# Optimization experiments

Hardware: AMD Instinct MI355X
Metric: run time of the kernel (lower is better)

## Reference

```python
import jax, jax.numpy as jnp
import numpy as np
import math

H, NH, NKV, HD, FF = 1024, 16, 4, 64, 4096
B, S = 2, 2048
EPS, THETA = 1e-6, 10000.0


def _rmsnorm(x, w, eps=EPS):
    v = jnp.mean(x.astype(jnp.float32) ** 2, axis=-1, keepdims=True)
    return (x.astype(jnp.float32) * jax.lax.rsqrt(v + eps)).astype(x.dtype) * w


def _rope_tables(seq_len, head_dim, theta=THETA):
    inv_freq = 1.0 / (theta ** (jnp.arange(0, head_dim, 2, dtype=jnp.float32) / head_dim))
    freqs = jnp.arange(seq_len, dtype=jnp.float32)[:, None] * inv_freq[None, :]
    emb = jnp.concatenate([freqs, freqs], axis=-1)  # [S, HD]
    return jnp.cos(emb), jnp.sin(emb)


def _rotate_half(x):
    x1, x2 = jnp.split(x, 2, axis=-1)
    return jnp.concatenate([-x2, x1], axis=-1)


def _apply_rope(x, cos, sin):
    # x: [B, h, S, HD]; cos/sin: [S, HD] broadcast over batch/heads
    return x * cos[None, None] + _rotate_half(x) * sin[None, None]


def setup_inputs() -> dict:
    key = jax.random.key(0)
    ks = jax.random.split(key, 12)
    std = 0.02
    return {
        "hidden_states": jax.random.normal(ks[0], (B, S, H), jnp.float32),
        "kv_states": jax.random.normal(ks[1], (B, S, H), jnp.float32),
        "attention_mask": jnp.zeros((B, 1, S, S), jnp.float32),
        "ln1_w": jnp.ones((H,), jnp.float32),
        "ln2_w": jnp.ones((H,), jnp.float32),
        "Wq": jax.random.normal(ks[2], (H, NH * HD), jnp.float32) * std,
        "Wk": jax.random.normal(ks[3], (H, NKV * HD), jnp.float32) * std,
        "Wv": jax.random.normal(ks[4], (H, NKV * HD), jnp.float32) * std,
        "Wo": jax.random.normal(ks[5], (NH * HD, H), jnp.float32) * std,
        "Wgate": jax.random.normal(ks[6], (H, FF), jnp.float32) * std,
        "Wup": jax.random.normal(ks[7], (H, FF), jnp.float32) * std,
        "Wdown": jax.random.normal(ks[8], (FF, H), jnp.float32) * std,
    }


def reference(hidden_states, kv_states, attention_mask, ln1_w, ln2_w,
              Wq, Wk, Wv, Wo, Wgate, Wup, Wdown):
    bsz, q_len, _ = hidden_states.shape
    k_len = kv_states.shape[1]

    residual = hidden_states
    h = _rmsnorm(hidden_states, ln1_w)   # input_layernorm on queries
    kv = _rmsnorm(kv_states, ln1_w)      # same norm applied to kv_states

    q = (h @ Wq).reshape(bsz, q_len, NH, HD).transpose(0, 2, 1, 3)    # [B,NH,Sq,HD]
    k = (kv @ Wk).reshape(bsz, k_len, NKV, HD).transpose(0, 2, 1, 3)  # [B,NKV,Sk,HD]
    v = (kv @ Wv).reshape(bsz, k_len, NKV, HD).transpose(0, 2, 1, 3)

    cos_q, sin_q = _rope_tables(q_len, HD)
    cos_k, sin_k = _rope_tables(k_len, HD)
    q = _apply_rope(q, cos_q, sin_q)
    k = _apply_rope(k, cos_k, sin_k)

    # repeat_kv: GQA expand to NH heads
    groups = NH // NKV
    k = jnp.repeat(k, groups, axis=1)
    v = jnp.repeat(v, groups, axis=1)

    scores = jnp.einsum("bhqd,bhkd->bhqk", q, k) / math.sqrt(HD)
    scores = scores + attention_mask  # additive mask [B,1,Sq,Sk]
    probs = jax.nn.softmax(scores.astype(jnp.float32), axis=-1).astype(q.dtype)
    attn = jnp.einsum("bhqk,bhkd->bhqd", probs, v)
    attn = attn.transpose(0, 2, 1, 3).reshape(bsz, q_len, NH * HD)
    attn = attn @ Wo

    hidden = residual + attn

    residual = hidden
    x = _rmsnorm(hidden, ln2_w)
    x = (jax.nn.silu(x @ Wgate) * (x @ Wup)) @ Wdown  # SwiGLU MLP
    return residual + x
```

## Files before the change

### kernel.cpp

```cpp
#include <hip/hip_runtime.h>
#include <math.h>

#define SS 2048

typedef __attribute__((ext_vector_type(8))) short s16x8;
typedef __attribute__((ext_vector_type(4))) float f32x4;
typedef __attribute__((ext_vector_type(16))) float f32x16;

__device__ __forceinline__ unsigned short f2bf(float f) {
  union { float f; unsigned u; } a; a.f = f;
  unsigned r = a.u + 0x7fffu + ((a.u >> 16) & 1u);
  return (unsigned short)(r >> 16);
}
__device__ __forceinline__ float bf2f(unsigned short b) {
  union { unsigned u; float f; } a; a.u = ((unsigned)b) << 16;
  return a.f;
}
__device__ __forceinline__ unsigned cvtpk(float a, float b) {
  unsigned d; asm("v_cvt_pk_bf16_f32 %0, %1, %2" : "=v"(d) : "v"(a), "v"(b)); return d;
}
__device__ __forceinline__ float fexp2(float x) {
  float r; asm("v_exp_f32 %0, %1" : "=v"(r) : "v"(x)); return r;
}
__device__ __forceinline__ void async16(void* lds, const void* g) {
  __builtin_amdgcn_global_load_lds(
      (const __attribute__((address_space(1))) unsigned int*)g,
      (__attribute__((address_space(3))) unsigned int*)lds, 16, 0, 0);
}
__device__ __forceinline__ f32x4 mfma_bf16(s16x8 a, s16x8 b, f32x4 c) {
  return __builtin_amdgcn_mfma_f32_16x16x32_bf16(a, b, c, 0, 0, 0);
}
__device__ __forceinline__ f32x16 mfma32(s16x8 a, s16x8 b, f32x16 c) {
  return __builtin_amdgcn_mfma_f32_32x32x16_bf16(a, b, c, 0, 0, 0);
}
__device__ __forceinline__ void xcd_swz(int& bx, int& by) {
  int nx = gridDim.x;
  int nwg = nx * gridDim.y;
  int bid = blockIdx.y * nx + blockIdx.x;
  int sid = (bid & 7) * (nwg >> 3) + (bid >> 3);
  bx = sid % nx; by = sid / nx;
}

__global__ __launch_bounds__(256) void k_transpose(const float* __restrict__ W,
                                                   const float* __restrict__ W2,
                                                   unsigned short* __restrict__ WT,
                                                   unsigned short* __restrict__ WT2,
                                                   int K, int N) {
  const float* Wp = blockIdx.z ? W2 : W;
  unsigned short* WTp = blockIdx.z ? WT2 : WT;
  __shared__ float tile[32][33];
  int t = threadIdx.x;
  int tx = t & 31, ty = t >> 5;
  int n0 = blockIdx.x * 32, k0 = blockIdx.y * 32;
#pragma unroll
  for (int i = 0; i < 4; ++i)
    tile[ty + 8 * i][tx] = Wp[(size_t)(k0 + ty + 8 * i) * N + n0 + tx];
  __syncthreads();
#pragma unroll
  for (int i = 0; i < 4; ++i)
    WTp[(size_t)(n0 + ty + 8 * i) * K + k0 + tx] = f2bf(tile[tx][ty + 8 * i]);
}

__global__ __launch_bounds__(256) void k_vtrans(const unsigned short* __restrict__ QKV,
                                                unsigned short* __restrict__ VT) {
  __shared__ unsigned short tile[32][33];
  int t = threadIdx.x, tx = t & 31, ty = t >> 5;
  int s0 = blockIdx.x * 32, d0 = blockIdx.y * 32;
  int bk = blockIdx.z; int b = bk >> 2, kvh = bk & 3;
#pragma unroll
  for (int i = 0; i < 4; ++i)
    tile[ty + 8 * i][tx] =
        QKV[((size_t)b * SS + s0 + ty + 8 * i) * 1536 + 1280 + kvh * 64 + d0 + tx];
  __syncthreads();
#pragma unroll
  for (int i = 0; i < 4; ++i)
    VT[((size_t)bk * 64 + d0 + ty + 8 * i) * SS + s0 + tx] = tile[tx][ty + 8 * i];
}

__global__ void k_rope_tables(float* __restrict__ cosT, float* __restrict__ sinT) {
  int idx = blockIdx.x * 256 + threadIdx.x;
  int s = idx >> 5, i = idx & 31;
  double ang = (double)s * pow(10000.0, -(double)(2 * i) / 64.0);
  cosT[idx] = (float)cos(ang);
  sinT[idx] = (float)sin(ang);
}

__global__ __launch_bounds__(256) void k_rmsnorm(const float* __restrict__ X,
                                                 const float* __restrict__ X2,
                                                 const float* __restrict__ Wt,
                                                 unsigned short* __restrict__ Y,
                                                 unsigned short* __restrict__ Y2) {
  int row = blockIdx.x, t = threadIdx.x;
  const float* Xp = X;
  unsigned short* Yp = Y;
  if (X2 && row >= 4096) { Xp = X2; Yp = Y2; row -= 4096; }
  float4 v = ((const float4*)Xp)[(size_t)row * 256 + t];
  float ssq = v.x * v.x + v.y * v.y + v.z * v.z + v.w * v.w;
#pragma unroll
  for (int m = 1; m < 64; m <<= 1) ssq += __shfl_xor(ssq, m);
  __shared__ float red[4];
  if ((t & 63) == 0) red[t >> 6] = ssq;
  __syncthreads();
  float sc = rsqrtf((red[0] + red[1] + red[2] + red[3]) * (1.0f / 1024.0f) + 1e-6f);
  float4 wv = ((const float4*)Wt)[t];
  ushort4 o;
  o.x = f2bf(v.x * sc * wv.x); o.y = f2bf(v.y * sc * wv.y);
  o.z = f2bf(v.z * sc * wv.z); o.w = f2bf(v.w * sc * wv.w);
  ((ushort4*)Yp)[(size_t)row * 256 + t] = o;
}

__global__ __launch_bounds__(256) void k_rope(unsigned short* __restrict__ X,
                                              const float* __restrict__ cosT,
                                              const float* __restrict__ sinT,
                                              int stride, int hbase) {
  int idx = blockIdx.x * 256 + threadIdx.x;
  int seg = idx & 7, tok = idx >> 3;
  int head = blockIdx.y + hbase;
  int s = tok & (SS - 1);
  int d0 = seg * 4;
  unsigned short* p = X + (size_t)tok * stride + head * 64;
  ushort4 lo = *(ushort4*)&p[d0];
  ushort4 hi = *(ushort4*)&p[d0 + 32];
  float4 cs = *(const float4*)&cosT[s * 32 + d0];
  float4 sn = *(const float4*)&sinT[s * 32 + d0];
  ushort4 olo, ohi;
  olo.x = f2bf(bf2f(lo.x) * cs.x - bf2f(hi.x) * sn.x);
  olo.y = f2bf(bf2f(lo.y) * cs.y - bf2f(hi.y) * sn.y);
  olo.z = f2bf(bf2f(lo.z) * cs.z - bf2f(hi.z) * sn.z);
  olo.w = f2bf(bf2f(lo.w) * cs.w - bf2f(hi.w) * sn.w);
  ohi.x = f2bf(bf2f(hi.x) * cs.x + bf2f(lo.x) * sn.x);
  ohi.y = f2bf(bf2f(hi.y) * cs.y + bf2f(lo.y) * sn.y);
  ohi.z = f2bf(bf2f(hi.z) * cs.z + bf2f(lo.z) * sn.z);
  ohi.w = f2bf(bf2f(hi.w) * cs.w + bf2f(lo.w) * sn.w);
  *(ushort4*)&p[d0] = olo;
  *(ushort4*)&p[d0 + 32] = ohi;
}

template <int EPI, int BN>
__global__ __launch_bounds__(256) void k_gemm(const unsigned short* __restrict__ A,
                                              const unsigned short* __restrict__ BT,
                                              int K, int ldc,
                                              unsigned short* Cb,
                                              float* __restrict__ Cf,
                                              const float* __restrict__ Res) {
  constexpr int NW = BN / 32;
  __shared__ __align__(16) unsigned short at[128 * 32];
  __shared__ __align__(16) unsigned short bt[BN * 32];
  int bx, by; xcd_swz(bx, by);
  int t = threadIdx.x, w = t >> 6, l = t & 63;
  int g = l >> 4, c = l & 15;
  int wm = w >> 1, wn = w & 1;
  f32x4 acc[4][NW] = {};
  const unsigned short* gA = A + (size_t)(by * 128 + (t >> 2)) * K + (t & 3) * 8;
  const unsigned short* gB = BT + (size_t)(bx * BN + (t >> 2)) * K + (t & 3) * 8;
  unsigned short* dA = &at[w * 512];
  unsigned short* dB = &bt[w * 512];
  const int nk = K >> 5;
  for (int kt = 0; kt < nk; ++kt) {
    async16(dA, gA);
    async16(dA + 2048, gA + (size_t)64 * K);
    async16(dB, gB);
    if (BN == 128) async16(dB + 2048, gB + (size_t)64 * K);
    gA += 32; gB += 32;
    __syncthreads();
    s16x8 af[4], bfr[NW];
#pragma unroll
    for (int m = 0; m < 4; ++m) af[m] = *(const s16x8*)&at[(wm * 64 + m * 16 + c) * 32 + g * 8];
#pragma unroll
    for (int n = 0; n < NW; ++n)
      bfr[n] = *(const s16x8*)&bt[(wn * (BN / 2) + n * 16 + c) * 32 + g * 8];
#pragma unroll
    for (int m = 0; m < 4; ++m)
#pragma unroll
      for (int n = 0; n < NW; ++n)
        acc[m][n] = mfma_bf16(af[m], bfr[n], acc[m][n]);
    __syncthreads();
  }
  size_t rb = (size_t)by * 128 + wm * 64;
  size_t cbase = (size_t)bx * BN + wn * (BN / 2);
#pragma unroll
  for (int m = 0; m < 4; ++m)
#pragma unroll
    for (int n = 0; n < NW; ++n)
#pragma unroll
      for (int r = 0; r < 4; ++r) {
        size_t row = rb + m * 16 + g * 4 + r;
        size_t col = cbase + n * 16 + c;
        float v = acc[m][n][r];
        if (EPI == 0) Cb[row * ldc + col] = f2bf(v);
        else Cf[row * ldc + col] = v + Res[row * ldc + col];
      }
}

__global__ __launch_bounds__(512) void k_gateup(const unsigned short* __restrict__ A,
                                                const unsigned short* __restrict__ BTg,
                                                const unsigned short* __restrict__ BTu,
                                                unsigned short* __restrict__ Cb) {
  __shared__ __align__(16) unsigned short at[128 * 32];
  __shared__ __align__(16) unsigned short bg[128 * 32];
  __shared__ __align__(16) unsigned short bu[128 * 32];
  int bx, by; xcd_swz(bx, by);
  int t = threadIdx.x, w = t >> 6, l = t & 63;
  int g = l >> 4, c = l & 15;
  int wm = w >> 2, wn = w & 3;
  f32x4 ag[4][2] = {}, au[4][2] = {};
  const unsigned short* gA = A + (size_t)(by * 128 + (t >> 2)) * 1024 + (t & 3) * 8;
  const unsigned short* gG = BTg + (size_t)(bx * 128 + (t >> 2)) * 1024 + (t & 3) * 8;
  const unsigned short* gU = BTu + (size_t)(bx * 128 + (t >> 2)) * 1024 + (t & 3) * 8;
  unsigned short* dA = &at[w * 512];
  unsigned short* dG = &bg[w * 512];
  unsigned short* dU = &bu[w * 512];
  for (int kt = 0; kt < 32; ++kt) {
    async16(dA, gA);
    async16(dG, gG);
    async16(dU, gU);
    gA += 32; gG += 32; gU += 32;
    __syncthreads();
    s16x8 af[4], bgf[2], buf_[2];
#pragma unroll
    for (int m = 0; m < 4; ++m) af[m] = *(const s16x8*)&at[(wm * 64 + m * 16 + c) * 32 + g * 8];
#pragma unroll
    for (int n = 0; n < 2; ++n) {
      bgf[n] = *(const s16x8*)&bg[(wn * 32 + n * 16 + c) * 32 + g * 8];
      buf_[n] = *(const s16x8*)&bu[(wn * 32 + n * 16 + c) * 32 + g * 8];
    }
#pragma unroll
    for (int m = 0; m < 4; ++m)
#pragma unroll
      for (int n = 0; n < 2; ++n) {
        ag[m][n] = mfma_bf16(af[m], bgf[n], ag[m][n]);
        au[m][n] = mfma_bf16(af[m], buf_[n], au[m][n]);
      }
    __syncthreads();
  }
  size_t rb = (size_t)by * 128 + wm * 64;
  size_t cb = (size_t)bx * 128 + wn * 32;
#pragma unroll
  for (int m = 0; m < 4; ++m)
#pragma unroll
    for (int n = 0; n < 2; ++n)
#pragma unroll
      for (int r = 0; r < 4; ++r) {
        size_t row = rb + m * 16 + g * 4 + r;
        size_t col = cb + n * 16 + c;
        float gv = ag[m][n][r], uv = au[m][n][r];
        Cb[row * 4096 + col] = f2bf(gv / (1.0f + __expf(-gv)) * uv);
      }
}

__global__ __launch_bounds__(256) void k_attn(const unsigned short* __restrict__ Q,
                                              const unsigned short* __restrict__ K,
                                              const unsigned short* __restrict__ VT,
                                              const float* __restrict__ mask,
                                              const float* __restrict__ cosT,
                                              const float* __restrict__ sinT,
                                              unsigned short* __restrict__ Out) {
  __shared__ __align__(16) unsigned short Ks[2][64 * 64];
  __shared__ __align__(16) unsigned short VTs[2][64 * 64];
  const float LOG2E = 1.44269504f;
  const float SCL2 = 0.125f * 1.44269504f;
  int t = threadIdx.x, w = t >> 6, l = t & 63;
  int q32 = l & 31, hi = l >> 5;
  int blk = blockIdx.x;
  int qt = blk & 63, kvh = (blk >> 6) & 3, b = blk >> 8;
  int head = kvh * 4 + w;
  size_t tokQ = (size_t)b * SS + qt * 32;

  s16x8 qfr[4];
#pragma unroll
  for (int d = 0; d < 4; ++d)
    qfr[d] = *(const s16x8*)&Q[(tokQ + q32) * 1536 + head * 64 + d * 16 + hi * 8];
  {
    int sp = qt * 32 + q32;
    const float* ct = cosT + sp * 32;
    const float* st = sinT + sp * 32;
#pragma unroll
    for (int d = 0; d < 2; ++d) {
      unsigned wlo[4], whi[4];
#pragma unroll
      for (int j = 0; j < 8; j += 2) {
        int f0 = d * 16 + hi * 8 + j;
        float c0 = ct[f0], s0_ = st[f0];
        float c1 = ct[f0 + 1], s1_ = st[f0 + 1];
        float lo0 = bf2f((unsigned short)qfr[d][j]);
        float hi0 = bf2f((unsigned short)qfr[d + 2][j]);
        float lo1 = bf2f((unsigned short)qfr[d][j + 1]);
        float hi1 = bf2f((unsigned short)qfr[d + 2][j + 1]);
        wlo[j >> 1] = cvtpk(lo0 * c0 - hi0 * s0_, lo1 * c1 - hi1 * s1_);
        whi[j >> 1] = cvtpk(hi0 * c0 + lo0 * s0_, hi1 * c1 + lo1 * s1_);
      }
      union { unsigned u[4]; s16x8 v; } a, b2;
#pragma unroll
      for (int i = 0; i < 4; ++i) { a.u[i] = wlo[i]; b2.u[i] = whi[i]; }
      qfr[d] = a.v;
      qfr[d + 2] = b2.v;
    }
  }
  const s16x8 one8 = {(short)0x3F80, (short)0x3F80, (short)0x3F80, (short)0x3F80,
                      (short)0x3F80, (short)0x3F80, (short)0x3F80, (short)0x3F80};

  int id0 = t, id1 = t + 256;
  int row0 = id0 >> 3, b80 = id0 & 7;
  int row1 = id1 >> 3, b81 = id1 & 7;
  int so0 = row0 * 64 + ((b80 ^ (row0 & 7)) << 3);
  int so1 = row1 * 64 + ((b81 ^ (row1 & 7)) << 3);
  const unsigned short* gK = K + (size_t)b * SS * 1536 + kvh * 64;
  const unsigned short* gV = VT + (size_t)(b * 4 + kvh) * 64 * SS;

  int4 rK0 = *(const int4*)(gK + (size_t)row0 * 1536 + b80 * 8);
  int4 rK1 = *(const int4*)(gK + (size_t)row1 * 1536 + b81 * 8);
  int4 rV0 = *(const int4*)(gV + (size_t)row0 * SS + b80 * 8);
  int4 rV1 = *(const int4*)(gV + (size_t)row1 * SS + b81 * 8);
  *(int4*)&Ks[0][so0] = rK0; *(int4*)&Ks[0][so1] = rK1;
  *(int4*)&VTs[0][so0] = rV0; *(int4*)&VTs[0][so1] = rV1;

  const float* mrowp = mask + (size_t)b * SS * SS + (size_t)(qt * 32 + q32) * SS + 4 * hi;
  float mc0[16], mc1[16];
#pragma unroll
  for (int j = 0; j < 4; ++j) {
    float4 v0 = *(const float4*)&mrowp[8 * j];
    float4 v1 = *(const float4*)&mrowp[32 + 8 * j];
    mc0[4 * j] = v0.x * LOG2E; mc0[4 * j + 1] = v0.y * LOG2E;
    mc0[4 * j + 2] = v0.z * LOG2E; mc0[4 * j + 3] = v0.w * LOG2E;
    mc1[4 * j] = v1.x * LOG2E; mc1[4 * j + 1] = v1.y * LOG2E;
    mc1[4 * j + 2] = v1.z * LOG2E; mc1[4 * j + 3] = v1.w * LOG2E;
  }

  f32x16 aco0 = {}, aco1 = {}, acl = {};
  float mrun = -1e30f;
  __syncthreads();

  for (int kt = 0; kt < 32; ++kt) {
    const unsigned short* Kc = Ks[kt & 1];
    const unsigned short* Vc = VTs[kt & 1];
    if (kt < 31) {
      int kb = (kt + 1) * 64;
      rK0 = *(const int4*)(gK + (size_t)(kb + row0) * 1536 + b80 * 8);
      rK1 = *(const int4*)(gK + (size_t)(kb + row1) * 1536 + b81 * 8);
      rV0 = *(const int4*)(gV + (size_t)row0 * SS + kb + b80 * 8);
      rV1 = *(const int4*)(gV + (size_t)row1 * SS + kb + b81 * 8);
    }
    f32x16 s0 = {}, s1 = {};
    __builtin_amdgcn_s_setprio(1);
#pragma unroll
    for (int d = 0; d < 4; ++d) {
      s16x8 ka = *(const s16x8*)&Kc[q32 * 64 + (((d * 2 + hi) ^ (q32 & 7)) << 3)];
      s0 = mfma32(ka, qfr[d], s0);
      int r2 = 32 + q32;
      s16x8 kb2 = *(const s16x8*)&Kc[r2 * 64 + (((d * 2 + hi) ^ (r2 & 7)) << 3)];
      s1 = mfma32(kb2, qfr[d], s1);
    }
    __builtin_amdgcn_s_setprio(0);
    float sv0[16], sv1[16];
#pragma unroll
    for (int r = 0; r < 16; ++r) {
      sv0[r] = s0[r] * SCL2 + mc0[r];
      sv1[r] = s1[r] * SCL2 + mc1[r];
    }
    {
      int nk = (kt < 31 ? kt + 1 : 31) * 64;
#pragma unroll
      for (int j = 0; j < 4; ++j) {
        float4 v0 = *(const float4*)&mrowp[nk + 8 * j];
        float4 v1 = *(const float4*)&mrowp[nk + 32 + 8 * j];
        mc0[4 * j] = v0.x * LOG2E; mc0[4 * j + 1] = v0.y * LOG2E;
        mc0[4 * j + 2] = v0.z * LOG2E; mc0[4 * j + 3] = v0.w * LOG2E;
        mc1[4 * j] = v1.x * LOG2E; mc1[4 * j + 1] = v1.y * LOG2E;
        mc1[4 * j + 2] = v1.z * LOG2E; mc1[4 * j + 3] = v1.w * LOG2E;
      }
    }
    float mx = sv0[0];
#pragma unroll
    for (int r = 1; r < 16; ++r) mx = fmaxf(mx, sv0[r]);
#pragma unroll
    for (int r = 0; r < 16; ++r) mx = fmaxf(mx, sv1[r]);
    mx = fmaxf(mx, __shfl_xor(mx, 32));
    if (__any(mx > mrun + 8.0f)) {
      float mnew = fmaxf(mrun, mx);
      float alpha = fexp2(mrun - mnew);
      mrun = mnew;
#pragma unroll
      for (int r = 0; r < 16; ++r) {
        float al = __shfl(alpha, (r & 3) + 8 * (r >> 2) + 4 * hi);
        aco0[r] *= al; aco1[r] *= al; acl[r] *= al;
      }
    }
    s16x8 pa[4];
#pragma unroll
    for (int ks = 0; ks < 2; ++ks) {
      float p[16];
      if (ks == 0) {
#pragma unroll
        for (int r = 0; r < 16; ++r) p[r] = fexp2(sv0[r] - mrun);
      } else {
#pragma unroll
        for (int r = 0; r < 16; ++r) p[r] = fexp2(sv1[r] - mrun);
      }
      unsigned w8[8];
#pragma unroll
      for (int i = 0; i < 8; ++i) w8[i] = cvtpk(p[2 * i], p[2 * i + 1]);
      unsigned sd0 = hi ? w8[0] : w8[2];
      unsigned sd1 = hi ? w8[1] : w8[3];
      unsigned sd2 = hi ? w8[4] : w8[6];
      unsigned sd3 = hi ? w8[5] : w8[7];
      unsigned rc0 = (unsigned)__shfl_xor((int)sd0, 32);
      unsigned rc1 = (unsigned)__shfl_xor((int)sd1, 32);
      unsigned rc2 = (unsigned)__shfl_xor((int)sd2, 32);
      unsigned rc3 = (unsigned)__shfl_xor((int)sd3, 32);
      union { int4 i; s16x8 v; } fa, fb;
      fa.i.x = hi ? rc0 : w8[0]; fa.i.y = hi ? rc1 : w8[1];
      fa.i.z = hi ? w8[2] : rc0; fa.i.w = hi ? w8[3] : rc1;
      fb.i.x = hi ? rc2 : w8[4]; fb.i.y = hi ? rc3 : w8[5];
      fb.i.z = hi ? w8[6] : rc2; fb.i.w = hi ? w8[7] : rc3;
      pa[2 * ks] = fa.v;
      pa[2 * ks + 1] = fb.v;
    }
    __builtin_amdgcn_s_setprio(1);
#pragma unroll
    for (int ks = 0; ks < 4; ++ks) {
      s16x8 va = *(const s16x8*)&Vc[q32 * 64 + (((ks * 2 + hi) ^ (q32 & 7)) << 3)];
      aco0 = mfma32(pa[ks], va, aco0);
      int r2 = 32 + q32;
      s16x8 vb2 = *(const s16x8*)&Vc[r2 * 64 + (((ks * 2 + hi) ^ (r2 & 7)) << 3)];
      aco1 = mfma32(pa[ks], vb2, aco1);
      acl = mfma32(pa[ks], one8, acl);
    }
    __builtin_amdgcn_s_setprio(0);
    if (kt < 31) {
      int nb = (kt + 1) & 1;
      *(int4*)&Ks[nb][so0] = rK0; *(int4*)&Ks[nb][so1] = rK1;
      *(int4*)&VTs[nb][so0] = rV0; *(int4*)&VTs[nb][so1] = rV1;
    }
    __syncthreads();
  }
#pragma unroll
  for (int r = 0; r < 16; ++r) {
    float inv = 1.0f / acl[r];
    size_t orow = tokQ + (r & 3) + 8 * (r >> 2) + 4 * hi;
    Out[orow * 1024 + head * 64 + q32] = f2bf(aco0[r] * inv);
    Out[orow * 1024 + head * 64 + 32 + q32] = f2bf(aco1[r] * inv);
  }
}

extern "C" void kernel_launch(void* const* d_in, const int* in_sizes, int n_in,
                              void* d_out, int out_size, void* d_ws, size_t ws_size,
                              hipStream_t stream) {
  (void)in_sizes; (void)n_in; (void)out_size; (void)ws_size;
  const float* hidden = (const float*)d_in[0];
  const float* kvst   = (const float*)d_in[1];
  const float* maskp  = (const float*)d_in[2];
  const float* ln1    = (const float*)d_in[3];
  const float* ln2    = (const float*)d_in[4];
  const float* Wq     = (const float*)d_in[5];
  const float* Wk     = (const float*)d_in[6];
  const float* Wv     = (const float*)d_in[7];
  const float* Wo     = (const float*)d_in[8];
  const float* Wg     = (const float*)d_in[9];
  const float* Wu     = (const float*)d_in[10];
  const float* Wd     = (const float*)d_in[11];
  float* out = (float*)d_out;

  char* ws = (char*)d_ws;
  size_t off = 0;
  auto alloc = [&](size_t bytes) { char* p = ws + off; off += (bytes + 255) & ~(size_t)255; return p; };
  unsigned short* WTqkv = (unsigned short*)alloc((size_t)1536 * 1024 * 2);
  unsigned short* WTo   = (unsigned short*)alloc((size_t)1024 * 1024 * 2);
  unsigned short* WTg   = (unsigned short*)alloc((size_t)4096 * 1024 * 2);
  unsigned short* WTu   = (unsigned short*)alloc((size_t)4096 * 1024 * 2);
  unsigned short* WTd   = (unsigned short*)alloc((size_t)1024 * 4096 * 2);
  float* cosT           = (float*)alloc((size_t)2048 * 32 * 4);
  float* sinT           = (float*)alloc((size_t)2048 * 32 * 4);
  unsigned short* hn    = (unsigned short*)alloc((size_t)4096 * 1024 * 2);
  unsigned short* kvn   = (unsigned short*)alloc((size_t)4096 * 1024 * 2);
  unsigned short* QKVb  = (unsigned short*)alloc((size_t)4096 * 1536 * 2);
  unsigned short* VTg   = (unsigned short*)alloc((size_t)8 * 64 * SS * 2);
  float* hid2           = (float*)alloc((size_t)4096 * 1024 * 4);
  unsigned short* inter = (unsigned short*)alloc((size_t)4096 * 4096 * 2);
  unsigned short* attnb = hn;
  unsigned short* h2n   = kvn;

  k_transpose<<<dim3(32, 32, 2), 256, 0, stream>>>(Wq, Wo, WTqkv, WTo, 1024, 1024);
  k_transpose<<<dim3(8, 32, 2), 256, 0, stream>>>(Wk, Wv, WTqkv + (size_t)1024 * 1024,
                                                  WTqkv + (size_t)1280 * 1024, 1024, 256);
  k_transpose<<<dim3(128, 32, 2), 256, 0, stream>>>(Wg, Wu, WTg, WTu, 1024, 4096);
  k_transpose<<<dim3(32, 128, 1), 256, 0, stream>>>(Wd, nullptr, WTd, nullptr, 4096, 1024);
  k_rope_tables<<<256, 256, 0, stream>>>(cosT, sinT);
  k_rmsnorm<<<8192, 256, 0, stream>>>(hidden, kvst, ln1, hn, kvn);
  k_gemm<0, 64><<<dim3(16, 32), 256, 0, stream>>>(hn, WTqkv, 1024, 1536, QKVb, nullptr, nullptr);
  k_gemm<0, 64><<<dim3(8, 32), 256, 0, stream>>>(kvn, WTqkv + (size_t)1024 * 1024, 1024, 1536,
                                                 QKVb + 1024, nullptr, nullptr);
  k_rope<<<dim3(128, 4), 256, 0, stream>>>(QKVb, cosT, sinT, 1536, 16);
  k_vtrans<<<dim3(64, 2, 8), 256, 0, stream>>>(QKVb, VTg);
  k_attn<<<512, 256, 0, stream>>>(QKVb, QKVb + 1024, VTg, maskp, cosT, sinT, attnb);
  k_gemm<1, 64><<<dim3(16, 32), 256, 0, stream>>>(attnb, WTo, 1024, 1024, nullptr, hid2, hidden);
  k_rmsnorm<<<4096, 256, 0, stream>>>(hid2, nullptr, ln2, h2n, nullptr);
  k_gateup<<<dim3(32, 32), 512, 0, stream>>>(h2n, WTg, WTu, inter);
  k_gemm<1, 64><<<dim3(16, 32), 256, 0, stream>>>(inter, WTd, 4096, 1024, nullptr, out, hid2);
}
```

Baseline: 326.0 us.

## Load K and V MFMA fragments directly from global memory, dropping LDS staging

The attention kernel stops staging K and V tiles through double-buffered shared memory and instead loads each wave's MFMA operand fragments straight from global memory into registers. K for the next tile is prefetched after the QK MFMAs, and V is loaded at the start of each iteration. This removes the LDS writes, LDS reads and per-iteration block barriers. In exchange, the four waves of a block (which share one KV head) each fetch the same K/V data separately, so global/L2 traffic rises fourfold, and the V loads have less time to cover their latency.

```diff
diff --git a/kernel.cpp b/kernel.cpp
--- a/kernel.cpp
+++ b/kernel.cpp
@@ -255,8 +255,6 @@
                                               const float* __restrict__ cosT,
                                               const float* __restrict__ sinT,
                                               unsigned short* __restrict__ Out) {
-  __shared__ __align__(16) unsigned short Ks[2][64 * 64];
-  __shared__ __align__(16) unsigned short VTs[2][64 * 64];
   const float LOG2E = 1.44269504f;
   const float SCL2 = 0.125f * 1.44269504f;
   int t = threadIdx.x, w = t >> 6, l = t & 63;
@@ -299,20 +297,12 @@
   const s16x8 one8 = {(short)0x3F80, (short)0x3F80, (short)0x3F80, (short)0x3F80,
                       (short)0x3F80, (short)0x3F80, (short)0x3F80, (short)0x3F80};
 
-  int id0 = t, id1 = t + 256;
-  int row0 = id0 >> 3, b80 = id0 & 7;
-  int row1 = id1 >> 3, b81 = id1 & 7;
-  int so0 = row0 * 64 + ((b80 ^ (row0 & 7)) << 3);
-  int so1 = row1 * 64 + ((b81 ^ (row1 & 7)) << 3);
   const unsigned short* gK = K + (size_t)b * SS * 1536 + kvh * 64;
   const unsigned short* gV = VT + (size_t)(b * 4 + kvh) * 64 * SS;
-
-  int4 rK0 = *(const int4*)(gK + (size_t)row0 * 1536 + b80 * 8);
-  int4 rK1 = *(const int4*)(gK + (size_t)row1 * 1536 + b81 * 8);
-  int4 rV0 = *(const int4*)(gV + (size_t)row0 * SS + b80 * 8);
-  int4 rV1 = *(const int4*)(gV + (size_t)row1 * SS + b81 * 8);
-  *(int4*)&Ks[0][so0] = rK0; *(int4*)&Ks[0][so1] = rK1;
-  *(int4*)&VTs[0][so0] = rV0; *(int4*)&VTs[0][so1] = rV1;
+  const unsigned short* kRow0 = gK + (size_t)q32 * 1536 + hi * 8;
+  const unsigned short* kRow1 = gK + (size_t)(q32 + 32) * 1536 + hi * 8;
+  const unsigned short* vRow0 = gV + (size_t)q32 * SS + hi * 8;
+  const unsigned short* vRow1 = gV + (size_t)(q32 + 32) * SS + hi * 8;
 
   const float* mrowp = mask + (size_t)b * SS * SS + (size_t)(qt * 32 + q32) * SS + 4 * hi;
   float mc0[16], mc1[16];
@@ -326,31 +316,44 @@
     mc1[4 * j + 2] = v1.z * LOG2E; mc1[4 * j + 3] = v1.w * LOG2E;
   }
 
+  s16x8 kA[4], kB[4];
+#pragma unroll
+  for (int d = 0; d < 4; ++d) {
+    kA[d] = *(const s16x8*)&kRow0[d * 16];
+    kB[d] = *(const s16x8*)&kRow1[d * 16];
+  }
+
   f32x16 aco0 = {}, aco1 = {}, acl = {};
   float mrun = -1e30f;
-  __syncthreads();
 
   for (int kt = 0; kt < 32; ++kt) {
-    const unsigned short* Kc = Ks[kt & 1];
-    const unsigned short* Vc = VTs[kt & 1];
-    if (kt < 31) {
-      int kb = (kt + 1) * 64;
-      rK0 = *(const int4*)(gK + (size_t)(kb + row0) * 1536 + b80 * 8);
-      rK1 = *(const int4*)(gK + (size_t)(kb + row1) * 1536 + b81 * 8);
-      rV0 = *(const int4*)(gV + (size_t)row0 * SS + kb + b80 * 8);
-      rV1 = *(const int4*)(gV + (size_t)row1 * SS + kb + b81 * 8);
+    s16x8 vA[4], vB[4];
+    {
+      const unsigned short* v0p = vRow0 + kt * 64;
+      const unsigned short* v1p = vRow1 + kt * 64;
+#pragma unroll
+      for (int ks = 0; ks < 4; ++ks) {
+        vA[ks] = *(const s16x8*)&v0p[ks * 16];
+        vB[ks] = *(const s16x8*)&v1p[ks * 16];
+      }
     }
     f32x16 s0 = {}, s1 = {};
     __builtin_amdgcn_s_setprio(1);
 #pragma unroll
     for (int d = 0; d < 4; ++d) {
-      s16x8 ka = *(const s16x8*)&Kc[q32 * 64 + (((d * 2 + hi) ^ (q32 & 7)) << 3)];
-      s0 = mfma32(ka, qfr[d], s0);
-      int r2 = 32 + q32;
-      s16x8 kb2 = *(const s16x8*)&Kc[r2 * 64 + (((d * 2 + hi) ^ (r2 & 7)) << 3)];
-      s1 = mfma32(kb2, qfr[d], s1);
+      s0 = mfma32(kA[d], qfr[d], s0);
+      s1 = mfma32(kB[d], qfr[d], s1);
     }
     __builtin_amdgcn_s_setprio(0);
+    if (kt < 31) {
+      const unsigned short* k0p = kRow0 + (size_t)(kt + 1) * 64 * 1536;
+      const unsigned short* k1p = kRow1 + (size_t)(kt + 1) * 64 * 1536;
+#pragma unroll
+      for (int d = 0; d < 4; ++d) {
+        kA[d] = *(const s16x8*)&k0p[d * 16];
+        kB[d] = *(const s16x8*)&k1p[d * 16];
+      }
+    }
     float sv0[16], sv1[16];
 #pragma unroll
     for (int r = 0; r < 16; ++r) {
@@ -418,20 +421,11 @@
     __builtin_amdgcn_s_setprio(1);
 #pragma unroll
     for (int ks = 0; ks < 4; ++ks) {
-      s16x8 va = *(const s16x8*)&Vc[q32 * 64 + (((ks * 2 + hi) ^ (q32 & 7)) << 3)];
-      aco0 = mfma32(pa[ks], va, aco0);
-      int r2 = 32 + q32;
-      s16x8 vb2 = *(const s16x8*)&Vc[r2 * 64 + (((ks * 2 + hi) ^ (r2 & 7)) << 3)];
-      aco1 = mfma32(pa[ks], vb2, aco1);
+      aco0 = mfma32(pa[ks], vA[ks], aco0);
+      aco1 = mfma32(pa[ks], vB[ks], aco1);
       acl = mfma32(pa[ks], one8, acl);
     }
     __builtin_amdgcn_s_setprio(0);
-    if (kt < 31) {
-      int nb = (kt + 1) & 1;
-      *(int4*)&Ks[nb][so0] = rK0; *(int4*)&Ks[nb][so1] = rK1;
-      *(int4*)&VTs[nb][so0] = rV0; *(int4*)&VTs[nb][so1] = rV1;
-    }
-    __syncthreads();
   }
 #pragma unroll
   for (int r = 0; r < 16; ++r) {
```

After: 427.3 us. +31.1%, slower.

## Double GEMM K-tile to 64 with XOR-swizzled LDS layout

Applied to the files above, without the earlier changes.

The projection GEMM and gate/up kernels now stage 64-wide K slices per iteration instead of 32. This halves the number of barrier pairs and loop iterations. The LDS rows grow to 64 elements, and the 16-byte chunk index is XOR-swizzled by row on both the global-load and fragment-read sides so reads avoid bank conflicts. LDS use doubles, which may reduce occupancy, especially in the gate/up kernel with three 16KB tiles.

```diff
diff --git a/kernel.cpp b/kernel.cpp
--- a/kernel.cpp
+++ b/kernel.cpp
@@ -144,36 +144,44 @@
                                               float* __restrict__ Cf,
                                               const float* __restrict__ Res) {
   constexpr int NW = BN / 32;
-  __shared__ __align__(16) unsigned short at[128 * 32];
-  __shared__ __align__(16) unsigned short bt[BN * 32];
+  __shared__ __align__(16) unsigned short at[128 * 64];
+  __shared__ __align__(16) unsigned short bt[BN * 64];
   int bx, by; xcd_swz(bx, by);
   int t = threadIdx.x, w = t >> 6, l = t & 63;
   int g = l >> 4, c = l & 15;
   int wm = w >> 1, wn = w & 1;
   f32x4 acc[4][NW] = {};
-  const unsigned short* gA = A + (size_t)(by * 128 + (t >> 2)) * K + (t & 3) * 8;
-  const unsigned short* gB = BT + (size_t)(bx * BN + (t >> 2)) * K + (t & 3) * 8;
+  int srow = t >> 3;
+  int scol = ((t & 7) ^ (srow & 7)) * 8;
+  const unsigned short* gA = A + (size_t)(by * 128 + srow) * K + scol;
+  const unsigned short* gB = BT + (size_t)(bx * BN + srow) * K + scol;
   unsigned short* dA = &at[w * 512];
   unsigned short* dB = &bt[w * 512];
-  const int nk = K >> 5;
+  const int nk = K >> 6;
   for (int kt = 0; kt < nk; ++kt) {
-    async16(dA, gA);
-    async16(dA + 2048, gA + (size_t)64 * K);
-    async16(dB, gB);
-    if (BN == 128) async16(dB + 2048, gB + (size_t)64 * K);
-    gA += 32; gB += 32;
+#pragma unroll
+    for (int j = 0; j < 4; ++j)
+      async16(dA + j * 2048, gA + (size_t)(32 * j) * K);
+#pragma unroll
+    for (int j = 0; j < BN / 32; ++j)
+      async16(dB + j * 2048, gB + (size_t)(32 * j) * K);
+    gA += 64; gB += 64;
     __syncthreads();
     s16x8 af[4], bfr[NW];
 #pragma unroll
-    for (int m = 0; m < 4; ++m) af[m] = *(const s16x8*)&at[(wm * 64 + m * 16 + c) * 32 + g * 8];
-#pragma unroll
-    for (int n = 0; n < NW; ++n)
-      bfr[n] = *(const s16x8*)&bt[(wn * (BN / 2) + n * 16 + c) * 32 + g * 8];
-#pragma unroll
-    for (int m = 0; m < 4; ++m)
+    for (int kk = 0; kk < 2; ++kk) {
+#pragma unroll
+      for (int m = 0; m < 4; ++m)
+        af[m] = *(const s16x8*)&at[(wm * 64 + m * 16 + c) * 64 + (((kk * 4 + g) ^ (c & 7)) << 3)];
 #pragma unroll
       for (int n = 0; n < NW; ++n)
-        acc[m][n] = mfma_bf16(af[m], bfr[n], acc[m][n]);
+        bfr[n] = *(const s16x8*)&bt[(wn * (BN / 2) + n * 16 + c) * 64 + (((kk * 4 + g) ^ (c & 7)) << 3)];
+#pragma unroll
+      for (int m = 0; m < 4; ++m)
+#pragma unroll
+        for (int n = 0; n < NW; ++n)
+          acc[m][n] = mfma_bf16(af[m], bfr[n], acc[m][n]);
+    }
     __syncthreads();
   }
   size_t rb = (size_t)by * 128 + wm * 64;
@@ -196,41 +204,51 @@
                                                 const unsigned short* __restrict__ BTg,
                                                 const unsigned short* __restrict__ BTu,
                                                 unsigned short* __restrict__ Cb) {
-  __shared__ __align__(16) unsigned short at[128 * 32];
-  __shared__ __align__(16) unsigned short bg[128 * 32];
-  __shared__ __align__(16) unsigned short bu[128 * 32];
+  __shared__ __align__(16) unsigned short at[128 * 64];
+  __shared__ __align__(16) unsigned short bg[128 * 64];
+  __shared__ __align__(16) unsigned short bu[128 * 64];
   int bx, by; xcd_swz(bx, by);
   int t = threadIdx.x, w = t >> 6, l = t & 63;
   int g = l >> 4, c = l & 15;
   int wm = w >> 2, wn = w & 3;
   f32x4 ag[4][2] = {}, au[4][2] = {};
-  const unsigned short* gA = A + (size_t)(by * 128 + (t >> 2)) * 1024 + (t & 3) * 8;
-  const unsigned short* gG = BTg + (size_t)(bx * 128 + (t >> 2)) * 1024 + (t & 3) * 8;
-  const unsigned short* gU = BTu + (size_t)(bx * 128 + (t >> 2)) * 1024 + (t & 3) * 8;
+  int srow = t >> 3;
+  int scol = ((t & 7) ^ (srow & 7)) * 8;
+  const unsigned short* gA = A + (size_t)(by * 128 + srow) * 1024 + scol;
+  const unsigned short* gG = BTg + (size_t)(bx * 128 + srow) * 1024 + scol;
+  const unsigned short* gU = BTu + (size_t)(bx * 128 + srow) * 1024 + scol;
   unsigned short* dA = &at[w * 512];
   unsigned short* dG = &bg[w * 512];
   unsigned short* dU = &bu[w * 512];
-  for (int kt = 0; kt < 32; ++kt) {
-    async16(dA, gA);
-    async16(dG, gG);
-    async16(dU, gU);
-    gA += 32; gG += 32; gU += 32;
+  for (int kt = 0; kt < 16; ++kt) {
+#pragma unroll
+    for (int j = 0; j < 2; ++j) {
+      async16(dA + j * 4096, gA + (size_t)(64 * j) * 1024);
+      async16(dG + j * 4096, gG + (size_t)(64 * j) * 1024);
+      async16(dU + j * 4096, gU + (size_t)(64 * j) * 1024);
+    }
+    gA += 64; gG += 64; gU += 64;
     __syncthreads();
     s16x8 af[4], bgf[2], buf_[2];
 #pragma unroll
-    for (int m = 0; m < 4; ++m) af[m] = *(const s16x8*)&at[(wm * 64 + m * 16 + c) * 32 + g * 8];
-#pragma unroll
-    for (int n = 0; n < 2; ++n) {
-      bgf[n] = *(const s16x8*)&bg[(wn * 32 + n * 16 + c) * 32 + g * 8];
-      buf_[n] = *(const s16x8*)&bu[(wn * 32 + n * 16 + c) * 32 + g * 8];
-    }
-#pragma unroll
-    for (int m = 0; m < 4; ++m)
+    for (int kk = 0; kk < 2; ++kk) {
+#pragma unroll
+      for (int m = 0; m < 4; ++m)
+        af[m] = *(const s16x8*)&at[(wm * 64 + m * 16 + c) * 64 + (((kk * 4 + g) ^ (c & 7)) << 3)];
 #pragma unroll
       for (int n = 0; n < 2; ++n) {
-        ag[m][n] = mfma_bf16(af[m], bgf[n], ag[m][n]);
-        au[m][n] = mfma_bf16(af[m], buf_[n], au[m][n]);
-      }
+        int roff = (wn * 32 + n * 16 + c) * 64 + (((kk * 4 + g) ^ (c & 7)) << 3);
+        bgf[n] = *(const s16x8*)&bg[roff];
+        buf_[n] = *(const s16x8*)&bu[roff];
+      }
+#pragma unroll
+      for (int m = 0; m < 4; ++m)
+#pragma unroll
+        for (int n = 0; n < 2; ++n) {
+          ag[m][n] = mfma_bf16(af[m], bgf[n], ag[m][n]);
+          au[m][n] = mfma_bf16(af[m], buf_[n], au[m][n]);
+        }
+    }
     __syncthreads();
   }
   size_t rb = (size_t)by * 128 + wm * 64;
```

Measured after the change: 292.2 us (median of 2 runs). 1.12x faster.
